# Performance work log

Measured on AMD Instinct MI355X. Metric: run time of the kernel, lower is better.

Reference implementation:

```python
import jax, jax.numpy as jnp
import numpy as np

B, C, N = 4, 16, 128
H_SET = 128   # set_layers[0]
D_OUT = 128   # channel_layers[0]


def setup_inputs() -> dict:
    key = jax.random.key(0)
    ks = jax.random.split(key, 7)
    x = jax.random.normal(ks[0], (B, C, N, N), dtype=jnp.float32)
    # phi: Linear(4 -> 128), ReLU, Linear(128 -> 2)
    W1 = jax.random.normal(ks[1], (H_SET, 4), dtype=jnp.float32) * 0.5
    b1 = jax.random.normal(ks[2], (H_SET,), dtype=jnp.float32) * 0.05
    W2 = jax.random.normal(ks[3], (2, H_SET), dtype=jnp.float32) * 0.1
    b2 = jax.random.normal(ks[4], (2,), dtype=jnp.float32) * 0.05
    # channel_fc: Conv2d(C -> 128, kernel 1) + ReLU  (1x1 conv == channel matmul)
    Wc = jax.random.normal(ks[5], (D_OUT, C), dtype=jnp.float32) * (1.0 / np.sqrt(C))
    bc = jax.random.normal(ks[6], (D_OUT,), dtype=jnp.float32) * 0.05
    return {"x": x, "W1": W1, "b1": b1, "W2": W2, "b2": b2, "Wc": Wc, "bc": bc}


def reference(x, W1, b1, W2, b2, Wc, bc):
    Bx, Cx, n, _ = x.shape
    ii = jnp.arange(n - 1)
    jj = jnp.arange(n)
    # group element g = i*n + j selects index pair (p, q) = (j, (j+i+1) mod n)
    p = jnp.broadcast_to(jj[None, :], (n - 1, n)).reshape(-1)        # (G,)
    q = ((jj[None, :] + ii[:, None] + 1) % n).reshape(-1)            # (G,)
    idx = jnp.stack([p, q], axis=-1)                                 # (G, 2)
    # gather 2x2 blocks: block[b,c,g] = x[b,c][[p,q]][:, [p,q]]
    block = x[:, :, idx[:, :, None], idx[:, None, :]]                # (B,C,G,2,2)
    v = block.reshape(Bx, Cx, -1, 4)                                 # (B,C,G,4)
    # phi: tiny per-element MLP 4 -> H -> 2
    h = jax.nn.relu(v @ W1.T + b1) @ W2.T + b2                       # (B,C,G,2)
    # scatter: off-diagonal entries get h[..., 1] at (p, q) (indices unique)
    out = jnp.zeros((Bx, Cx, n, n), x.dtype).at[:, :, p, q].set(h[..., 1])
    # diagonal: diag[j] = sum_i h[:, :, i*n + j, 0]
    diag = h[..., 0].reshape(Bx, Cx, n - 1, n).sum(axis=2)           # (B,C,n)
    ar = jnp.arange(n)
    out = out.at[:, :, ar, ar].add(diag)
    # coeff: 1 off-diagonal, 1/(n-1) on diagonal
    eye = jnp.eye(n, dtype=x.dtype)
    coeff = (1.0 - eye) + eye * (1.0 / (n - 1))
    out = out * coeff
    # channel_fc: 1x1 conv + ReLU
    y = jax.nn.relu(jnp.einsum('bcnm,dc->bdnm', out, Wc) + bc[None, :, None, None])
    return y
```

## Files before the change

kernel.cpp:

```cpp
#include <hip/hip_runtime.h>

#define NN 128
#define CCH 16
#define BB 4
#define GP 2
#define HID 128
#define DOUT 128

__global__ __launch_bounds__(512, 2) void fused_rey(
    const float* __restrict__ x, const float* __restrict__ W1,
    const float* __restrict__ b1, const float* __restrict__ W2,
    const float* __restrict__ b2, const float* __restrict__ Wc,
    const float* __restrict__ bc, float* __restrict__ y)
{
    __shared__ float4 w1s[HID];
    __shared__ float4 wbs[HID];
    __shared__ float  wcs[DOUT][CCH];
    __shared__ float  bcs[DOUT];
    __shared__ float  s_out[CCH][GP][NN];
    __shared__ float  s_part[8][4][GP];

    const int t   = threadIdx.x;
    const int bid = blockIdx.x;
    const int pg  = bid & 63;
    const int b   = bid >> 6;
    const int p0  = pg * GP;
    const int q   = t & 127;
    const int cq  = t >> 7;

    if (t < HID) {
        w1s[t] = reinterpret_cast<const float4*>(W1)[t];
        wbs[t] = make_float4(b1[t], W2[t], W2[HID + t], 0.f);
        bcs[t] = bc[t];
    }
    reinterpret_cast<float4*>(wcs)[t] = reinterpret_cast<const float4*>(Wc)[t];

    const float bb0 = b2[0], bb1 = b2[1];
    float x_pp[4][GP], x_pq[4][GP], x_qp[4][GP], x_qq[4];
    #pragma unroll
    for (int j = 0; j < 4; ++j) {
        const int c = cq + 4 * j;
        const float* xm = x + ((size_t)(b * CCH + c) << 14);
        x_qq[j] = xm[q * (NN + 1)];
        const float2 qp = *reinterpret_cast<const float2*>(&xm[q * NN + p0]);
        x_qp[j][0] = qp.x; x_qp[j][1] = qp.y;
        #pragma unroll
        for (int pp = 0; pp < GP; ++pp) {
            x_pp[j][pp] = xm[(p0 + pp) * (NN + 1)];
            x_pq[j][pp] = xm[(p0 + pp) * NN + q];
        }
    }
    float h0[4][GP], h1[4][GP];
    #pragma unroll
    for (int j = 0; j < 4; ++j)
        #pragma unroll
        for (int pp = 0; pp < GP; ++pp) { h0[j][pp] = bb0; h1[j][pp] = bb1; }

    __syncthreads();

    #pragma unroll 4
    for (int k = 0; k < HID; ++k) {
        const float4 w  = w1s[k];
        const float4 wb = wbs[k];
        #pragma unroll
        for (int j = 0; j < 4; ++j) {
            const float s = fmaf(w.w, x_qq[j], wb.x);
            #pragma unroll
            for (int pp = 0; pp < GP; ++pp) {
                float hd = fmaf(w.x, x_pp[j][pp], s);
                hd = fmaf(w.y, x_pq[j][pp], hd);
                hd = fmaf(w.z, x_qp[j][pp], hd);
                hd = fmaxf(hd, 0.f);
                h0[j][pp] = fmaf(wb.y, hd, h0[j][pp]);
                h1[j][pp] = fmaf(wb.z, hd, h1[j][pp]);
            }
        }
    }

    #pragma unroll
    for (int j = 0; j < 4; ++j) {
        const int c = cq + 4 * j;
        #pragma unroll
        for (int pp = 0; pp < GP; ++pp) {
            s_out[c][pp][q] = h1[j][pp];
            if (q == p0 + pp) h0[j][pp] = 0.f;
        }
    }

    const int wv = t >> 6;
    #pragma unroll
    for (int j = 0; j < 4; ++j)
        #pragma unroll
        for (int pp = 0; pp < GP; ++pp) {
            float v = h0[j][pp];
            for (int off = 32; off > 0; off >>= 1)
                v += __shfl_down(v, off, 64);
            if ((t & 63) == 0) s_part[wv][j][pp] = v;
        }
    __syncthreads();
    if (t < 32) {
        const int cq2 = t >> 3, j2 = (t >> 1) & 3, pp2 = t & 1;
        const int c2 = cq2 + 4 * j2;
        const float v = (s_part[cq2 * 2][j2][pp2] + s_part[cq2 * 2 + 1][j2][pp2])
                        * (1.0f / (NN - 1));
        s_out[c2][pp2][p0 + pp2] = v;
    }
    __syncthreads();

    const int m0   = (t & 31) * 4;
    const int dgrp = t >> 5;
    #pragma unroll
    for (int pp = 0; pp < GP; ++pp) {
        float4 r[CCH];
        #pragma unroll
        for (int c = 0; c < CCH; ++c)
            r[c] = *reinterpret_cast<const float4*>(&s_out[c][pp][m0]);
        #pragma unroll
        for (int dd = 0; dd < 8; ++dd) {
            const int d = dgrp * 8 + dd;
            const float4 wr0 = reinterpret_cast<const float4*>(&wcs[d][0])[0];
            const float4 wr1 = reinterpret_cast<const float4*>(&wcs[d][0])[1];
            const float4 wr2 = reinterpret_cast<const float4*>(&wcs[d][0])[2];
            const float4 wr3 = reinterpret_cast<const float4*>(&wcs[d][0])[3];
            const float wv16[16] = { wr0.x, wr0.y, wr0.z, wr0.w,
                                     wr1.x, wr1.y, wr1.z, wr1.w,
                                     wr2.x, wr2.y, wr2.z, wr2.w,
                                     wr3.x, wr3.y, wr3.z, wr3.w };
            const float bcv = bcs[d];
            float4 acc = make_float4(bcv, bcv, bcv, bcv);
            #pragma unroll
            for (int c = 0; c < CCH; ++c) {
                acc.x = fmaf(wv16[c], r[c].x, acc.x);
                acc.y = fmaf(wv16[c], r[c].y, acc.y);
                acc.z = fmaf(wv16[c], r[c].z, acc.z);
                acc.w = fmaf(wv16[c], r[c].w, acc.w);
            }
            acc.x = fmaxf(acc.x, 0.f);
            acc.y = fmaxf(acc.y, 0.f);
            acc.z = fmaxf(acc.z, 0.f);
            acc.w = fmaxf(acc.w, 0.f);
            float* yp = y + ((((size_t)(b * DOUT + d)) * NN + (p0 + pp)) * NN + m0);
            *reinterpret_cast<float4*>(yp) = acc;
        }
    }
}

extern "C" void kernel_launch(void* const* d_in, const int* in_sizes, int n_in,
                              void* d_out, int out_size, void* d_ws, size_t ws_size,
                              hipStream_t stream) {
    const float* x  = (const float*)d_in[0];
    const float* W1 = (const float*)d_in[1];
    const float* b1 = (const float*)d_in[2];
    const float* W2 = (const float*)d_in[3];
    const float* b2 = (const float*)d_in[4];
    const float* Wc = (const float*)d_in[5];
    const float* bc = (const float*)d_in[6];
    float* y = (float*)d_out;

    dim3 grid(BB * (NN / GP));
    fused_rey<<<grid, 512, 0, stream>>>(x, W1, b1, W2, b2, Wc, bc, y);
}
```

Measured before the change: 39.70 us.

## Process one row per block and read weights directly from global memory

Drops the two-rows-per-block grouping, so the grid doubles to one block per (batch, row). The shared-memory staging of W1/b1/W2/Wc/bc is removed; weights are read straight from global memory as wave-uniform, cached loads. The 1x1 conv epilogue now gives each wave 16 output channels with float2 stores. This frees shared memory and registers for higher occupancy, but it loses the reuse of x_qq and the weights across two rows and adds more global weight loads.

```diff
diff --git a/kernel.cpp b/kernel.cpp
--- a/kernel.cpp
+++ b/kernel.cpp
@@ -3,145 +3,106 @@
 #define NN 128
 #define CCH 16
 #define BB 4
-#define GP 2
 #define HID 128
 #define DOUT 128
 
-__global__ __launch_bounds__(512, 2) void fused_rey(
+__global__ __launch_bounds__(512, 4) void fused_rey(
     const float* __restrict__ x, const float* __restrict__ W1,
     const float* __restrict__ b1, const float* __restrict__ W2,
     const float* __restrict__ b2, const float* __restrict__ Wc,
     const float* __restrict__ bc, float* __restrict__ y)
 {
-    __shared__ float4 w1s[HID];
-    __shared__ float4 wbs[HID];
-    __shared__ float  wcs[DOUT][CCH];
-    __shared__ float  bcs[DOUT];
-    __shared__ float  s_out[CCH][GP][NN];
-    __shared__ float  s_part[8][4][GP];
+    __shared__ float s_out[CCH][NN];
+    __shared__ float s_part[8][4];
 
     const int t   = threadIdx.x;
     const int bid = blockIdx.x;
-    const int pg  = bid & 63;
-    const int b   = bid >> 6;
-    const int p0  = pg * GP;
+    const int p   = bid & 127;
+    const int b   = bid >> 7;
     const int q   = t & 127;
     const int cq  = t >> 7;
-
-    if (t < HID) {
-        w1s[t] = reinterpret_cast<const float4*>(W1)[t];
-        wbs[t] = make_float4(b1[t], W2[t], W2[HID + t], 0.f);
-        bcs[t] = bc[t];
-    }
-    reinterpret_cast<float4*>(wcs)[t] = reinterpret_cast<const float4*>(Wc)[t];
+    const int wv  = t >> 6;
 
     const float bb0 = b2[0], bb1 = b2[1];
-    float x_pp[4][GP], x_pq[4][GP], x_qp[4][GP], x_qq[4];
+
+    float x_pp[4], x_pq[4], x_qp[4], x_qq[4];
     #pragma unroll
     for (int j = 0; j < 4; ++j) {
         const int c = cq + 4 * j;
         const float* xm = x + ((size_t)(b * CCH + c) << 14);
+        x_pp[j] = xm[p * (NN + 1)];
+        x_pq[j] = xm[p * NN + q];
+        x_qp[j] = xm[q * NN + p];
         x_qq[j] = xm[q * (NN + 1)];
-        const float2 qp = *reinterpret_cast<const float2*>(&xm[q * NN + p0]);
-        x_qp[j][0] = qp.x; x_qp[j][1] = qp.y;
-        #pragma unroll
-        for (int pp = 0; pp < GP; ++pp) {
-            x_pp[j][pp] = xm[(p0 + pp) * (NN + 1)];
-            x_pq[j][pp] = xm[(p0 + pp) * NN + q];
-        }
     }
-    float h0[4][GP], h1[4][GP];
+
+    float h0[4], h1[4];
     #pragma unroll
-    for (int j = 0; j < 4; ++j)
-        #pragma unroll
-        for (int pp = 0; pp < GP; ++pp) { h0[j][pp] = bb0; h1[j][pp] = bb1; }
-
-    __syncthreads();
+    for (int j = 0; j < 4; ++j) { h0[j] = bb0; h1[j] = bb1; }
 
     #pragma unroll 4
     for (int k = 0; k < HID; ++k) {
-        const float4 w  = w1s[k];
-        const float4 wb = wbs[k];
+        const float4 w  = reinterpret_cast<const float4*>(W1)[k];
+        const float b1k = b1[k];
+        const float w20 = W2[k];
+        const float w21 = W2[HID + k];
         #pragma unroll
         for (int j = 0; j < 4; ++j) {
-            const float s = fmaf(w.w, x_qq[j], wb.x);
-            #pragma unroll
-            for (int pp = 0; pp < GP; ++pp) {
-                float hd = fmaf(w.x, x_pp[j][pp], s);
-                hd = fmaf(w.y, x_pq[j][pp], hd);
-                hd = fmaf(w.z, x_qp[j][pp], hd);
-                hd = fmaxf(hd, 0.f);
-                h0[j][pp] = fmaf(wb.y, hd, h0[j][pp]);
-                h1[j][pp] = fmaf(wb.z, hd, h1[j][pp]);
-            }
+            float hd = fmaf(w.x, x_pp[j], b1k);
+            hd = fmaf(w.y, x_pq[j], hd);
+            hd = fmaf(w.z, x_qp[j], hd);
+            hd = fmaf(w.w, x_qq[j], hd);
+            hd = fmaxf(hd, 0.f);
+            h0[j] = fmaf(w20, hd, h0[j]);
+            h1[j] = fmaf(w21, hd, h1[j]);
         }
     }
 
     #pragma unroll
     for (int j = 0; j < 4; ++j) {
         const int c = cq + 4 * j;
-        #pragma unroll
-        for (int pp = 0; pp < GP; ++pp) {
-            s_out[c][pp][q] = h1[j][pp];
-            if (q == p0 + pp) h0[j][pp] = 0.f;
-        }
+        s_out[c][q] = h1[j];
+        if (q == p) h0[j] = 0.f;
     }
 
-    const int wv = t >> 6;
     #pragma unroll
-    for (int j = 0; j < 4; ++j)
-        #pragma unroll
-        for (int pp = 0; pp < GP; ++pp) {
-            float v = h0[j][pp];
-            for (int off = 32; off > 0; off >>= 1)
-                v += __shfl_down(v, off, 64);
-            if ((t & 63) == 0) s_part[wv][j][pp] = v;
-        }
+    for (int j = 0; j < 4; ++j) {
+        float v = h0[j];
+        for (int off = 32; off > 0; off >>= 1)
+            v += __shfl_down(v, off, 64);
+        if ((t & 63) == 0) s_part[wv][j] = v;
+    }
     __syncthreads();
-    if (t < 32) {
-        const int cq2 = t >> 3, j2 = (t >> 1) & 3, pp2 = t & 1;
+    if (t < 16) {
+        const int cq2 = t >> 2, j2 = t & 3;
         const int c2 = cq2 + 4 * j2;
-        const float v = (s_part[cq2 * 2][j2][pp2] + s_part[cq2 * 2 + 1][j2][pp2])
-                        * (1.0f / (NN - 1));
-        s_out[c2][pp2][p0 + pp2] = v;
+        s_out[c2][p] = (s_part[2 * cq2][j2] + s_part[2 * cq2 + 1][j2])
+                       * (1.0f / (NN - 1));
     }
     __syncthreads();
 
-    const int m0   = (t & 31) * 4;
-    const int dgrp = t >> 5;
+    const int lane = t & 63;
+    const int m0 = lane * 2;
+    float2 r[CCH];
     #pragma unroll
-    for (int pp = 0; pp < GP; ++pp) {
-        float4 r[CCH];
+    for (int c = 0; c < CCH; ++c)
+        r[c] = *reinterpret_cast<const float2*>(&s_out[c][m0]);
+
+    #pragma unroll
+    for (int dd = 0; dd < 16; ++dd) {
+        const int d = wv * 16 + dd;
+        const float bcv = bc[d];
+        float2 acc = { bcv, bcv };
         #pragma unroll
-        for (int c = 0; c < CCH; ++c)
-            r[c] = *reinterpret_cast<const float4*>(&s_out[c][pp][m0]);
-        #pragma unroll
-        for (int dd = 0; dd < 8; ++dd) {
-            const int d = dgrp * 8 + dd;
-            const float4 wr0 = reinterpret_cast<const float4*>(&wcs[d][0])[0];
-            const float4 wr1 = reinterpret_cast<const float4*>(&wcs[d][0])[1];
-            const float4 wr2 = reinterpret_cast<const float4*>(&wcs[d][0])[2];
-            const float4 wr3 = reinterpret_cast<const float4*>(&wcs[d][0])[3];
-            const float wv16[16] = { wr0.x, wr0.y, wr0.z, wr0.w,
-                                     wr1.x, wr1.y, wr1.z, wr1.w,
-                                     wr2.x, wr2.y, wr2.z, wr2.w,
-                                     wr3.x, wr3.y, wr3.z, wr3.w };
-            const float bcv = bcs[d];
-            float4 acc = make_float4(bcv, bcv, bcv, bcv);
-            #pragma unroll
-            for (int c = 0; c < CCH; ++c) {
-                acc.x = fmaf(wv16[c], r[c].x, acc.x);
-                acc.y = fmaf(wv16[c], r[c].y, acc.y);
-                acc.z = fmaf(wv16[c], r[c].z, acc.z);
-                acc.w = fmaf(wv16[c], r[c].w, acc.w);
-            }
-            acc.x = fmaxf(acc.x, 0.f);
-            acc.y = fmaxf(acc.y, 0.f);
-            acc.z = fmaxf(acc.z, 0.f);
-            acc.w = fmaxf(acc.w, 0.f);
-            float* yp = y + ((((size_t)(b * DOUT + d)) * NN + (p0 + pp)) * NN + m0);
-            *reinterpret_cast<float4*>(yp) = acc;
+        for (int c = 0; c < CCH; ++c) {
+            const float wcv = Wc[d * CCH + c];
+            acc.x = fmaf(wcv, r[c].x, acc.x);
+            acc.y = fmaf(wcv, r[c].y, acc.y);
         }
+        acc.x = fmaxf(acc.x, 0.f);
+        acc.y = fmaxf(acc.y, 0.f);
+        float* yp = y + ((((size_t)(b * DOUT + d)) * NN + p) * NN + m0);
+        *reinterpret_cast<float2*>(yp) = acc;
     }
 }
 
@@ -157,6 +118,6 @@
     const float* bc = (const float*)d_in[6];
     float* y = (float*)d_out;
 
-    dim3 grid(BB * (NN / GP));
+    dim3 grid(BB * NN);
     fused_rey<<<grid, 512, 0, stream>>>(x, W1, b1, W2, b2, Wc, bc, y);
 }
```

After: 41.26 us. 1.04x slower.
